# Optimization experiments

Hardware: AMD Instinct MI355X
Metric: run time of the kernel (lower is better)

The kernel has to match this reference:

```python
import jax, jax.numpy as jnp
import numpy as np

LSTM_SIZE = 512
MEM_SIZE = 2048
MEM_DIM = 256
NB_READS = 4
GAMMA = 0.95
EPS = 1e-8
B = 64
IN_RAW = 256
IN_TOTAL = IN_RAW + NB_READS * MEM_SIZE  # 8448
PARAM_DIM = (2 * MEM_DIM + 1) * NB_READS  # 2052


def setup_inputs() -> dict:
    key = jax.random.key(0)
    ks = jax.random.split(key, 8)
    s = 0.02
    return {
        "x": jax.random.normal(ks[0], (B, IN_RAW), jnp.float32),
        "M": jax.random.normal(ks[1], (B, MEM_SIZE, MEM_DIM), jnp.float32),
        "wu": jax.random.uniform(ks[2], (B, MEM_SIZE), jnp.float32),
        "wr": jax.random.uniform(ks[3], (B, NB_READS * MEM_SIZE), jnp.float32),
        "h0": jnp.zeros((LSTM_SIZE,), jnp.float32),
        "c0": jnp.zeros((LSTM_SIZE,), jnp.float32),
        "W_ih": jax.random.normal(ks[4], (4 * LSTM_SIZE, IN_TOTAL), jnp.float32) * s,
        "W_hh": jax.random.normal(ks[5], (4 * LSTM_SIZE, LSTM_SIZE), jnp.float32) * s,
        "b_ih": jnp.zeros((4 * LSTM_SIZE,), jnp.float32),
        "b_hh": jnp.zeros((4 * LSTM_SIZE,), jnp.float32),
        "W_p": jax.random.normal(ks[6], (PARAM_DIM, LSTM_SIZE), jnp.float32) * s,
        "b_p": jax.random.uniform(ks[7], (PARAM_DIM,), jnp.float32, -0.1, 0.1),
    }


def _lstm_scan(x_seq, h0, c0, W_ih, W_hh, b):
    # torch treats the 2-D input as an unbatched sequence of length B:
    # the recurrence runs across the batch axis with a single shared state.
    xW = x_seq @ W_ih.T + b  # [B, 4H] precomputed input contribution

    def step(carry, xw):
        h, c = carry
        g = xw + h @ W_hh.T
        i, f, gg, o = jnp.split(g, 4)
        c = jax.nn.sigmoid(f) * c + jax.nn.sigmoid(i) * jnp.tanh(gg)
        h = jax.nn.sigmoid(o) * jnp.tanh(c)
        return (h, c), h

    (hf, cf), hs = jax.lax.scan(step, (h0, c0), xW)
    return hs, hf, cf


def reference(x, M, wu, wr, h0, c0, W_ih, W_hh, b_ih, b_hh, W_p, b_p):
    ctrl_in = jnp.concatenate([x, wr], axis=-1)  # [B, IN_TOTAL]
    hs, hf, cf = _lstm_scan(ctrl_in, h0, c0, W_ih, W_hh, b_ih + b_hh)
    param = hs @ W_p.T + b_p  # [B, PARAM_DIM]

    nd = NB_READS * MEM_DIM
    k = jnp.tanh(param[:, :nd]).reshape(B, NB_READS, MEM_DIM)
    a = jnp.tanh(param[:, nd:2 * nd]).reshape(B, NB_READS, MEM_DIM)
    sig_alpha = jax.nn.sigmoid(param[:, -NB_READS:])  # [B, R]

    # least_used: topk(wu, k=MEM_SIZE) == full descending sort of indices
    order = jnp.argsort(-wu, axis=-1)  # [B, MEM_SIZE]
    lu_idx = order[:, -1]  # least used slot
    wlu = jax.nn.one_hot(order[:, -NB_READS:], MEM_SIZE, dtype=M.dtype).sum(1)  # [B, N]

    # read head addressing: cosine similarity softmax
    ip = jnp.einsum('brd,bnd->brn', k, M)  # [B, R, N]
    k_norm = jnp.sqrt(jnp.sum(k * k, -1))[:, :, None]
    M_norm = jnp.sqrt(jnp.sum(M * M, -1))[:, None, :]
    wr_t = jax.nn.softmax(ip / (k_norm * M_norm + EPS), axis=-1)  # [B, R, N]

    # write head addressing
    wr_prev3 = wr.reshape(B, NB_READS, MEM_SIZE)
    sa = sig_alpha[:, :, None]
    ww_t = sa * wr_prev3 + (1.0 - sa) * wlu[:, None, :]  # [B, R, N]

    wu_t = GAMMA * wu + wr_t.sum(1) + ww_t.sum(1)  # [B, N]

    erase = 1.0 - jax.nn.one_hot(lu_idx, MEM_SIZE, dtype=M.dtype)  # [B, N]
    M_t = M * erase[:, :, None] + jnp.einsum('brn,brd->bnd', ww_t, a)  # [B, N, D]
    r_t = jnp.einsum('brn,bnd->brd', wr_t, M_t).reshape(B, nd)  # [B, R*D]

    return jnp.concatenate([hs, r_t], axis=-1)  # [B, LSTM+R*D]
```

## Files before the change

### kernel.cpp

```cpp
#include <hip/hip_runtime.h>
#include <hip/hip_bf16.h>

#define BB 64
#define IN_RAW_ 256
#define KIN_ 8448
#define WRW 8192
#define PD_ 2052
#define XW_KS 11
#define XW_CH 768

__global__ __launch_bounds__(256) void k_xw_partial(
    const float* __restrict__ x, const float* __restrict__ wr,
    const float* __restrict__ Wih, float* __restrict__ xwp) {
  const int jb = blockIdx.x & 31;
  const int ks = blockIdx.x >> 5;
  const int j0 = jb << 6;
  const int k0 = ks * XW_CH;
  __shared__ __align__(16) float As[32][68];
  __shared__ __align__(16) float Bs[32][68];
  const int tid = threadIdx.x;
  const int ti = tid & 15, tj = tid >> 4;
  const int lt = tid >> 2, lq = tid & 3;
  float acc[4][4];
#pragma unroll
  for (int i = 0; i < 4; ++i)
#pragma unroll
    for (int j = 0; j < 4; ++j) acc[i][j] = 0.f;
  for (int kc = 0; kc < XW_CH; kc += 32) {
    __syncthreads();
    const int kb = k0 + kc + (lq << 3);
    float va[8], vb[8];
    if (kb < IN_RAW_) {
      const float* p = x + lt * IN_RAW_ + kb;
#pragma unroll
      for (int u = 0; u < 8; ++u) va[u] = p[u];
    } else {
      const float* p = wr + (size_t)lt * WRW + (kb - IN_RAW_);
#pragma unroll
      for (int u = 0; u < 8; ++u) va[u] = p[u];
    }
    {
      const float* p = Wih + (size_t)(j0 + lt) * KIN_ + kb;
#pragma unroll
      for (int u = 0; u < 8; ++u) vb[u] = p[u];
    }
#pragma unroll
    for (int u = 0; u < 8; ++u) As[(lq << 3) + u][lt] = va[u];
#pragma unroll
    for (int u = 0; u < 8; ++u) Bs[(lq << 3) + u][lt] = vb[u];
    __syncthreads();
#pragma unroll
    for (int kk = 0; kk < 32; ++kk) {
      const float4 a4 = *(const float4*)&As[kk][ti << 2];
      const float4 b4 = *(const float4*)&Bs[kk][tj << 2];
      const float av[4] = {a4.x, a4.y, a4.z, a4.w};
      const float bv[4] = {b4.x, b4.y, b4.z, b4.w};
#pragma unroll
      for (int i = 0; i < 4; ++i)
#pragma unroll
        for (int j = 0; j < 4; ++j) acc[i][j] = fmaf(av[i], bv[j], acc[i][j]);
    }
  }
#pragma unroll
  for (int i = 0; i < 4; ++i) {
    const int t = (ti << 2) + i;
    float* dst = xwp + ((size_t)(ks * BB + t) << 11) + j0 + (tj << 2);
    dst[0] = acc[i][0]; dst[1] = acc[i][1]; dst[2] = acc[i][2]; dst[3] = acc[i][3];
  }
}

__global__ __launch_bounds__(256) void k_xw_reduce(
    const float* __restrict__ xwp, const float* __restrict__ bih,
    const float* __restrict__ bhh, float* __restrict__ xw) {
  const int e = blockIdx.x * 256 + threadIdx.x;
  const int j = e & 2047;
  float s = bih[j] + bhh[j];
#pragma unroll
  for (int ks = 0; ks < XW_KS; ++ks) s += xwp[(size_t)ks * 131072 + e];
  xw[e] = s;
}

__global__ __launch_bounds__(64, 1) void k_scan(
    const float* __restrict__ xw, const float* __restrict__ Whh,
    const float* __restrict__ h0, const float* __restrict__ c0,
    unsigned long long* __restrict__ ht, float* __restrict__ out,
    const float* __restrict__ wu, int* __restrict__ t4) {
  const int W = blockIdx.x;
  const int l = threadIdx.x;
  if (W >= 128) {
    const int b = W - 128;
    float val[32];
#pragma unroll
    for (int i = 0; i < 32; ++i) val[i] = wu[(b << 11) + (i << 6) + l];
    for (int pick = 0; pick < 4; ++pick) {
      float bv = 3.4e38f; int bi = -1;
#pragma unroll
      for (int i = 0; i < 32; ++i) {
        const int n = (i << 6) + l;
        const float v = val[i];
        if (v < bv || (v == bv && n > bi)) { bv = v; bi = n; }
      }
#pragma unroll
      for (int s = 1; s < 64; s <<= 1) {
        const float ov = __shfl_xor(bv, s);
        const int oi = __shfl_xor(bi, s);
        if (ov < bv || (ov == bv && oi > bi)) { bv = ov; bi = oi; }
      }
      if (l == 0) t4[(b << 2) + pick] = bi;
      if ((bi & 63) == l) val[bi >> 6] = 3.4e38f;
    }
    return;
  }
  const int d = l & 3;
  const int jj = (W << 2) + d;
  float wreg[16][8];
#pragma unroll
  for (int r = 0; r < 16; ++r) {
    const int row = ((r >> 2) << 9) + (W << 2) + (r & 3);
    const float* p = Whh + ((size_t)row << 9) + (l << 3);
#pragma unroll
    for (int u = 0; u < 8; ++u) wreg[r][u] = p[u];
  }
  float c = 0.f;
  if (l < 4) c = c0[jj];
  float h[8];
#pragma unroll
  for (int u = 0; u < 8; ++u) h[u] = h0[(l << 3) + u];

  for (int t = 0; t < 64; ++t) {
    float xv0 = 0, xv1 = 0, xv2 = 0, xv3 = 0;
    if (l < 4) {
      const float* xp = xw + (t << 11) + jj;
      xv0 = xp[0]; xv1 = xp[512]; xv2 = xp[1024]; xv3 = xp[1536];
    }
    if (t > 0) {
      const unsigned long long* hp = ht + (t << 9) + (l << 3);
      unsigned long long va[8], vb[8];
#pragma unroll
      for (int u = 0; u < 8; ++u)
        va[u] = __hip_atomic_load(hp + u, __ATOMIC_RELAXED, __HIP_MEMORY_SCOPE_AGENT);
      for (;;) {
#pragma unroll
        for (int u = 0; u < 8; ++u)
          vb[u] = __hip_atomic_load(hp + u, __ATOMIC_RELAXED, __HIP_MEMORY_SCOPE_AGENT);
        bool ra = true;
#pragma unroll
        for (int u = 0; u < 8; ++u) ra &= ((unsigned)(va[u] >> 32) == (unsigned)t);
        if (ra) break;
#pragma unroll
        for (int u = 0; u < 8; ++u)
          va[u] = __hip_atomic_load(hp + u, __ATOMIC_RELAXED, __HIP_MEMORY_SCOPE_AGENT);
        bool rb_ = true;
#pragma unroll
        for (int u = 0; u < 8; ++u) rb_ &= ((unsigned)(vb[u] >> 32) == (unsigned)t);
        if (rb_) {
#pragma unroll
          for (int u = 0; u < 8; ++u) va[u] = vb[u];
          break;
        }
      }
#pragma unroll
      for (int u = 0; u < 8; ++u) h[u] = __uint_as_float((unsigned)va[u]);
    }
    float pr[16];
#pragma unroll
    for (int r = 0; r < 16; ++r) {
      float s = 0.f;
#pragma unroll
      for (int u = 0; u < 8; ++u) s = fmaf(wreg[r][u], h[u], s);
      pr[r] = s;
    }
    float v8[8], v4[4], v2[2], v1;
    {
      const bool b0 = (l & 1) != 0;
#pragma unroll
      for (int j = 0; j < 8; ++j) {
        const float keep = b0 ? pr[2 * j + 1] : pr[2 * j];
        const float send = b0 ? pr[2 * j] : pr[2 * j + 1];
        v8[j] = keep + __shfl_xor(send, 1);
      }
    }
    {
      const bool b1 = (l & 2) != 0;
#pragma unroll
      for (int j = 0; j < 4; ++j) {
        const float keep = b1 ? v8[2 * j + 1] : v8[2 * j];
        const float send = b1 ? v8[2 * j] : v8[2 * j + 1];
        v4[j] = keep + __shfl_xor(send, 2);
      }
    }
    {
      const bool b2 = (l & 4) != 0;
#pragma unroll
      for (int j = 0; j < 2; ++j) {
        const float keep = b2 ? v4[2 * j + 1] : v4[2 * j];
        const float send = b2 ? v4[2 * j] : v4[2 * j + 1];
        v2[j] = keep + __shfl_xor(send, 4);
      }
    }
    {
      const bool b3 = (l & 8) != 0;
      const float keep = b3 ? v2[1] : v2[0];
      const float send = b3 ? v2[0] : v2[1];
      v1 = keep + __shfl_xor(send, 8);
    }
    v1 += __shfl_xor(v1, 16);
    v1 += __shfl_xor(v1, 32);
    const float gi_ = __shfl(v1, d);
    const float gf_ = __shfl(v1, d + 4);
    const float gg_ = __shfl(v1, d + 8);
    const float go_ = __shfl(v1, d + 12);
    if (l < 4) {
      const float gi = gi_ + xv0;
      const float gf = gf_ + xv1;
      const float gg = gg_ + xv2;
      const float go = go_ + xv3;
      const float si = 1.f / (1.f + __expf(-gi));
      const float sf = 1.f / (1.f + __expf(-gf));
      const float so = 1.f / (1.f + __expf(-go));
      const float tg = 2.f / (1.f + __expf(-2.f * gg)) - 1.f;
      c = sf * c + si * tg;
      const float tc = 2.f / (1.f + __expf(-2.f * c)) - 1.f;
      const float hnew = so * tc;
      const unsigned long long pk =
          ((unsigned long long)(unsigned)(t + 1) << 32) |
          (unsigned long long)__float_as_uint(hnew);
      __hip_atomic_store(ht + ((t + 1) << 9) + jj, pk, __ATOMIC_RELAXED,
                         __HIP_MEMORY_SCOPE_AGENT);
      out[t * 1536 + jj] = hnew;
    }
  }
}

__global__ __launch_bounds__(256) void k_param(
    const float* __restrict__ outbuf, const float* __restrict__ Wp,
    const float* __restrict__ bp, float* __restrict__ km,
    float* __restrict__ am, float* __restrict__ sa) {
  const int j0 = blockIdx.x << 6;
  __shared__ __align__(16) float As[32][68];
  __shared__ __align__(16) float Bs[32][68];
  const int tid = threadIdx.x;
  const int ti = tid & 15, tj = tid >> 4;
  const int lt = tid >> 2, lq = tid & 3;
  float acc[4][4];
#pragma unroll
  for (int i = 0; i < 4; ++i)
#pragma unroll
    for (int j = 0; j < 4; ++j) acc[i][j] = 0.f;
  for (int kc = 0; kc < 512; kc += 32) {
    __syncthreads();
    const int kb = kc + (lq << 3);
    float va[8], vb[8];
    {
      const float* p = outbuf + lt * 1536 + kb;
#pragma unroll
      for (int u = 0; u < 8; ++u) va[u] = p[u];
    }
    const int brow = j0 + lt;
    if (brow < PD_) {
      const float* p = Wp + (size_t)brow * 512 + kb;
#pragma unroll
      for (int u = 0; u < 8; ++u) vb[u] = p[u];
    } else {
#pragma unroll
      for (int u = 0; u < 8; ++u) vb[u] = 0.f;
    }
#pragma unroll
    for (int u = 0; u < 8; ++u) As[(lq << 3) + u][lt] = va[u];
#pragma unroll
    for (int u = 0; u < 8; ++u) Bs[(lq << 3) + u][lt] = vb[u];
    __syncthreads();
#pragma unroll
    for (int kk = 0; kk < 32; ++kk) {
      const float4 a4 = *(const float4*)&As[kk][ti << 2];
      const float4 b4 = *(const float4*)&Bs[kk][tj << 2];
      const float av[4] = {a4.x, a4.y, a4.z, a4.w};
      const float bv[4] = {b4.x, b4.y, b4.z, b4.w};
#pragma unroll
      for (int i = 0; i < 4; ++i)
#pragma unroll
        for (int j = 0; j < 4; ++j) acc[i][j] = fmaf(av[i], bv[j], acc[i][j]);
    }
  }
#pragma unroll
  for (int i = 0; i < 4; ++i) {
    const int b = (ti << 2) + i;
#pragma unroll
    for (int j = 0; j < 4; ++j) {
      const int col = j0 + (tj << 2) + j;
      if (col < PD_) {
        const float v = acc[i][j] + bp[col];
        if (col < 1024) km[(b << 10) + col] = tanhf(v);
        else if (col < 2048) am[(b << 10) + col - 1024] = tanhf(v);
        else sa[(b << 2) + col - 2048] = 1.f / (1.f + expf(-v));
      }
    }
  }
}

__global__ __launch_bounds__(256) void k_ip(
    const float* __restrict__ M, const float* __restrict__ km,
    float* __restrict__ ip, float* __restrict__ mn) {
  const int b = blockIdx.x >> 4;
  const int nb = blockIdx.x & 15;
  const int n0 = nb << 7;
  const int tid = threadIdx.x;
  const int wv = tid >> 6, l = tid & 63;
  const int q = l >> 4, l16 = l & 15;
  float kr[4][16];
#pragma unroll
  for (int r = 0; r < 4; ++r)
#pragma unroll
    for (int cc = 0; cc < 4; ++cc) {
      const float4 kv = *(const float4*)(km + (((b << 2) + r) << 8) + (cc << 6) + (l16 << 2));
      kr[r][(cc << 2) + 0] = kv.x; kr[r][(cc << 2) + 1] = kv.y;
      kr[r][(cc << 2) + 2] = kv.z; kr[r][(cc << 2) + 3] = kv.w;
    }
  for (int it = 0; it < 8; ++it) {
    const int n = n0 + (wv << 5) + (it << 2) + q;
    const float* mrow = M + (((size_t)b << 11) + n) * 256;
    float s[4] = {0.f, 0.f, 0.f, 0.f};
    float sm = 0.f;
#pragma unroll
    for (int cc = 0; cc < 4; ++cc) {
      const float4 m4 = *(const float4*)(mrow + (cc << 6) + (l16 << 2));
      const float mv[4] = {m4.x, m4.y, m4.z, m4.w};
#pragma unroll
      for (int e = 0; e < 4; ++e) {
        sm = fmaf(mv[e], mv[e], sm);
#pragma unroll
        for (int r = 0; r < 4; ++r) s[r] = fmaf(kr[r][(cc << 2) + e], mv[e], s[r]);
      }
    }
#pragma unroll
    for (int r = 0; r < 4; ++r) {
      float v = s[r];
      v += __shfl_xor(v, 1); v += __shfl_xor(v, 2); v += __shfl_xor(v, 4); v += __shfl_xor(v, 8);
      s[r] = v;
    }
    sm += __shfl_xor(sm, 1); sm += __shfl_xor(sm, 2); sm += __shfl_xor(sm, 4); sm += __shfl_xor(sm, 8);
    if (l16 == 0) {
      const size_t base = ((size_t)b) << 13;
      ip[base + n] = s[0];
      ip[base + 2048 + n] = s[1];
      ip[base + 4096 + n] = s[2];
      ip[base + 6144 + n] = s[3];
      mn[(b << 11) + n] = sqrtf(sm);
    }
  }
}

__global__ __launch_bounds__(512) void k_softmax(
    const float* __restrict__ ip, const float* __restrict__ mn_g,
    const float* __restrict__ sa_g, const float* __restrict__ wr_in,
    const int* __restrict__ t4, const float* __restrict__ am,
    const float* __restrict__ M, const float* __restrict__ km,
    float* __restrict__ wrt, float* __restrict__ rb) {
  const int b = blockIdx.x;
  const int tid = threadIdx.x;
  const int wv = tid >> 6, l = tid & 63;
  __shared__ float lam[4][2048];
  __shared__ float mnl[2048];
  __shared__ float Sd[16];
  __shared__ float t4s[4];
  __shared__ float Sl[16];
#pragma unroll
  for (int i = 0; i < 4; ++i) mnl[tid + (i << 9)] = mn_g[(b << 11) + tid + (i << 9)];
  __syncthreads();
  if (wv < 4) {
    const int r = wv;
    const float* kp = km + (b << 10) + (r << 8);
    float sq = 0.f;
#pragma unroll
    for (int i = 0; i < 4; ++i) { const float v = kp[l + (i << 6)]; sq = fmaf(v, v, sq); }
    sq += __shfl_xor(sq, 1);  sq += __shfl_xor(sq, 2);  sq += __shfl_xor(sq, 4);
    sq += __shfl_xor(sq, 8);  sq += __shfl_xor(sq, 16); sq += __shfl_xor(sq, 32);
    const float kn = sqrtf(sq);
    const float* ipr = ip + (((size_t)b) << 13) + ((size_t)r << 11);
    float mx = -3.4e38f;
#pragma unroll 4
    for (int i = 0; i < 32; ++i) {
      const int n = l + (i << 6);
      const float v = ipr[n] / fmaf(kn, mnl[n], 1e-8f);
      lam[r][n] = v;
      mx = fmaxf(mx, v);
    }
    mx = fmaxf(mx, __shfl_xor(mx, 1));  mx = fmaxf(mx, __shfl_xor(mx, 2));
    mx = fmaxf(mx, __shfl_xor(mx, 4));  mx = fmaxf(mx, __shfl_xor(mx, 8));
    mx = fmaxf(mx, __shfl_xor(mx, 16)); mx = fmaxf(mx, __shfl_xor(mx, 32));
    float sum = 0.f;
#pragma unroll 4
    for (int i = 0; i < 32; ++i) {
      const int n = l + (i << 6);
      const float e = expf(lam[r][n] - mx);
      lam[r][n] = e;
      sum += e;
    }
    sum += __shfl_xor(sum, 1);  sum += __shfl_xor(sum, 2);  sum += __shfl_xor(sum, 4);
    sum += __shfl_xor(sum, 8);  sum += __shfl_xor(sum, 16); sum += __shfl_xor(sum, 32);
    const float inv = 1.f / sum;
#pragma unroll 4
    for (int i = 0; i < 32; ++i) {
      const int n = l + (i << 6);
      const float w_ = lam[r][n] * inv;
      lam[r][n] = w_;
      wrt[(((size_t)(b << 2) + r) << 11) + n] = w_;
    }
  }
  __syncthreads();
#pragma unroll
  for (int j = 0; j < 2; ++j) {
    const int pr = (wv << 1) + j;
    const int r = pr >> 2, qq = pr & 3;
    const float* wp = wr_in + (size_t)b * WRW + (qq << 11);
    float s = 0.f;
#pragma unroll 4
    for (int i = 0; i < 32; ++i) {
      const int n = l + (i << 6);
      s = fmaf(lam[r][n], wp[n], s);
    }
    s += __shfl_xor(s, 1);  s += __shfl_xor(s, 2);  s += __shfl_xor(s, 4);
    s += __shfl_xor(s, 8);  s += __shfl_xor(s, 16); s += __shfl_xor(s, 32);
    if (l == 0) Sd[pr] = s;
  }
  if (tid < 4) {
    float s = 0.f;
#pragma unroll
    for (int ii = 0; ii < 4; ++ii) s += lam[tid][t4[(b << 2) + ii]];
    t4s[tid] = s;
  }
  __syncthreads();
  if (tid < 16) {
    const int r = tid >> 2, qq = tid & 3;
    const float sv = sa_g[(b << 2) + qq];
    Sl[tid] = sv * Sd[tid] + (1.f - sv) * t4s[r];
  }
  __syncthreads();
  const int luv = t4[b << 2];
#pragma unroll
  for (int i = 0; i < 2; ++i) {
    const int e = tid + (i << 9);
    const int r = e >> 8, d = e & 255;
    const float mlu = M[(((size_t)b << 11) + luv) * 256 + d];
    float v = -lam[r][luv] * mlu;
#pragma unroll
    for (int qq = 0; qq < 4; ++qq)
      v = fmaf(Sl[(r << 2) + qq], am[(((b << 2) + qq) << 8) + d], v);
    rb[(((b << 2) + r) << 8) + d] = v;
  }
}

__global__ __launch_bounds__(256) void k_rt_partial(
    const float* __restrict__ wrt, const float* __restrict__ M,
    float* __restrict__ rtp) {
  const int b = blockIdx.x >> 3;
  const int ns = blockIdx.x & 7;
  const int tid = threadIdx.x;
  const int wv = tid >> 6, l = tid & 63;
  __shared__ float wl[4][256];
  __shared__ float4 red[4][4][64];
#pragma unroll
  for (int i = 0; i < 4; ++i) {
    const int e = tid + (i << 8);
    const int r = e >> 8, nn = e & 255;
    wl[r][nn] = wrt[(((size_t)(b << 2) + r) << 11) + (ns << 8) + nn];
  }
  __syncthreads();
  float4 acc[4];
#pragma unroll
  for (int r = 0; r < 4; ++r) acc[r] = make_float4(0.f, 0.f, 0.f, 0.f);
  for (int it = 0; it < 64; ++it) {
    const int nl = (wv << 6) + it;
    const float4 m4 =
        *(const float4*)(M + (((size_t)b << 11) + (ns << 8) + nl) * 256 + (l << 2));
#pragma unroll
    for (int r = 0; r < 4; ++r) {
      const float w_ = wl[r][nl];
      acc[r].x = fmaf(w_, m4.x, acc[r].x);
      acc[r].y = fmaf(w_, m4.y, acc[r].y);
      acc[r].z = fmaf(w_, m4.z, acc[r].z);
      acc[r].w = fmaf(w_, m4.w, acc[r].w);
    }
  }
#pragma unroll
  for (int r = 0; r < 4; ++r) red[wv][r][l] = acc[r];
  __syncthreads();
  if (wv == 0) {
#pragma unroll
    for (int r = 0; r < 4; ++r) {
      float4 s = red[0][r][l];
#pragma unroll
      for (int w2 = 1; w2 < 4; ++w2) {
        const float4 o = red[w2][r][l];
        s.x += o.x; s.y += o.y; s.z += o.z; s.w += o.w;
      }
      *(float4*)(rtp + ((size_t)(((ns << 6) + b) << 2) + r) * 256 + (l << 2)) = s;
    }
  }
}

__global__ __launch_bounds__(256) void k_rt_finish(
    const float* __restrict__ rtp, const float* __restrict__ rb,
    float* __restrict__ out) {
  const int b = blockIdx.x;
  const int tid = threadIdx.x;
#pragma unroll
  for (int i = 0; i < 4; ++i) {
    const int e = tid + (i << 8);
    float s = rb[(b << 10) + e];
#pragma unroll
    for (int ns = 0; ns < 8; ++ns) s += rtp[((size_t)(((ns << 6) + b)) << 10) + e];
    out[b * 1536 + 512 + e] = s;
  }
}

extern "C" void kernel_launch(void* const* d_in, const int* in_sizes, int n_in,
                              void* d_out, int out_size, void* d_ws, size_t ws_size,
                              hipStream_t stream) {
  (void)in_sizes; (void)n_in; (void)out_size;
  const float* x   = (const float*)d_in[0];
  const float* M   = (const float*)d_in[1];
  const float* wu  = (const float*)d_in[2];
  const float* wr  = (const float*)d_in[3];
  const float* h0  = (const float*)d_in[4];
  const float* c0  = (const float*)d_in[5];
  const float* Wih = (const float*)d_in[6];
  const float* Whh = (const float*)d_in[7];
  const float* bih = (const float*)d_in[8];
  const float* bhh = (const float*)d_in[9];
  const float* Wp  = (const float*)d_in[10];
  const float* bp  = (const float*)d_in[11];
  float* out = (float*)d_out;
  char* ws = (char*)d_ws;
  if (ws_size < 14161920u) return;

  float* xwp = (float*)(ws + 0);
  float* xw  = (float*)(ws + 5767168);
  float* km  = (float*)(ws + 6291456);
  float* am  = (float*)(ws + 6553600);
  float* sa  = (float*)(ws + 6815744);
  int*   t4  = (int*)(ws + 6816768);
  float* ipb = (float*)(ws + 6817792);
  float* mnb = (float*)(ws + 8914944);
  float* wrt = (float*)(ws + 9439232);
  float* rb  = (float*)(ws + 11536384);
  float* rtp = (float*)(ws + 11798528);
  unsigned long long* ht = (unsigned long long*)(ws + 13895680);

  hipMemsetAsync(ht, 0, 65 * 512 * 8, stream);
  hipLaunchKernelGGL(k_xw_partial, dim3(352), dim3(256), 0, stream, x, wr, Wih, xwp);
  hipLaunchKernelGGL(k_xw_reduce, dim3(512), dim3(256), 0, stream, xwp, bih, bhh, xw);
  hipLaunchKernelGGL(k_scan, dim3(192), dim3(64), 0, stream,
                     xw, Whh, h0, c0, ht, out, wu, t4);
  hipLaunchKernelGGL(k_param, dim3(33), dim3(256), 0, stream, out, Wp, bp, km, am, sa);
  hipLaunchKernelGGL(k_ip, dim3(1024), dim3(256), 0, stream, M, km, ipb, mnb);
  hipLaunchKernelGGL(k_softmax, dim3(64), dim3(512), 0, stream,
                     ipb, mnb, sa, wr, t4, am, M, km, wrt, rb);
  hipLaunchKernelGGL(k_rt_partial, dim3(512), dim3(256), 0, stream, wrt, M, rtp);
  hipLaunchKernelGGL(k_rt_finish, dim3(64), dim3(256), 0, stream, rtp, rb, out);
}
```

Measured before the change: 284.5 us.

## Move memory-norm computation into scan side blocks and fuse readout into softmax

The per-slot memory norms are now computed by 256 extra blocks launched alongside the sequential LSTM scan kernel, so that work hides under the latency-bound recurrence instead of sitting in k_ip. The softmax kernel now also performs the weighted read over M directly from shared-memory weights and writes the output. This removes the wrt/rb/rtp intermediates and two kernel launches. The risk is that the fused readout runs with only 64 blocks, each streaming 2 MB of M, which may underuse the GPU compared with the earlier 512-block split. The extra scan blocks could also contend with the scan's spin-synchronising blocks.

```diff
diff --git a/kernel.cpp b/kernel.cpp
--- a/kernel.cpp
+++ b/kernel.cpp
@@ -84,9 +84,30 @@
     const float* __restrict__ xw, const float* __restrict__ Whh,
     const float* __restrict__ h0, const float* __restrict__ c0,
     unsigned long long* __restrict__ ht, float* __restrict__ out,
-    const float* __restrict__ wu, int* __restrict__ t4) {
+    const float* __restrict__ wu, int* __restrict__ t4,
+    const float* __restrict__ M, float* __restrict__ mn) {
   const int W = blockIdx.x;
   const int l = threadIdx.x;
+  if (W >= 192) {
+    const int idx = W - 192;
+    const int g0 = idx << 9;
+    const int sub = l >> 4, c16 = l & 15;
+    for (int it = 0; it < 128; ++it) {
+      const int g = g0 + (it << 2) + sub;
+      const float* mrow = M + (size_t)g * 256;
+      float sq = 0.f;
+#pragma unroll
+      for (int ch = 0; ch < 4; ++ch) {
+        const float4 m4 = *(const float4*)(mrow + (ch << 6) + (c16 << 2));
+        sq = fmaf(m4.x, m4.x, sq); sq = fmaf(m4.y, m4.y, sq);
+        sq = fmaf(m4.z, m4.z, sq); sq = fmaf(m4.w, m4.w, sq);
+      }
+      sq += __shfl_xor(sq, 1); sq += __shfl_xor(sq, 2);
+      sq += __shfl_xor(sq, 4); sq += __shfl_xor(sq, 8);
+      if (c16 == 0) mn[g] = sqrtf(sq);
+    }
+    return;
+  }
   if (W >= 128) {
     const int b = W - 128;
     float val[32];
@@ -300,7 +321,7 @@
 
 __global__ __launch_bounds__(256) void k_ip(
     const float* __restrict__ M, const float* __restrict__ km,
-    float* __restrict__ ip, float* __restrict__ mn) {
+    float* __restrict__ ip) {
   const int b = blockIdx.x >> 4;
   const int nb = blockIdx.x & 15;
   const int n0 = nb << 7;
@@ -320,14 +341,12 @@
     const int n = n0 + (wv << 5) + (it << 2) + q;
     const float* mrow = M + (((size_t)b << 11) + n) * 256;
     float s[4] = {0.f, 0.f, 0.f, 0.f};
-    float sm = 0.f;
 #pragma unroll
     for (int cc = 0; cc < 4; ++cc) {
       const float4 m4 = *(const float4*)(mrow + (cc << 6) + (l16 << 2));
       const float mv[4] = {m4.x, m4.y, m4.z, m4.w};
 #pragma unroll
       for (int e = 0; e < 4; ++e) {
-        sm = fmaf(mv[e], mv[e], sm);
 #pragma unroll
         for (int r = 0; r < 4; ++r) s[r] = fmaf(kr[r][(cc << 2) + e], mv[e], s[r]);
       }
@@ -338,24 +357,22 @@
       v += __shfl_xor(v, 1); v += __shfl_xor(v, 2); v += __shfl_xor(v, 4); v += __shfl_xor(v, 8);
       s[r] = v;
     }
-    sm += __shfl_xor(sm, 1); sm += __shfl_xor(sm, 2); sm += __shfl_xor(sm, 4); sm += __shfl_xor(sm, 8);
     if (l16 == 0) {
       const size_t base = ((size_t)b) << 13;
       ip[base + n] = s[0];
       ip[base + 2048 + n] = s[1];
       ip[base + 4096 + n] = s[2];
       ip[base + 6144 + n] = s[3];
-      mn[(b << 11) + n] = sqrtf(sm);
-    }
-  }
-}
-
-__global__ __launch_bounds__(512) void k_softmax(
+    }
+  }
+}
+
+__global__ __launch_bounds__(512) void k_smrt(
     const float* __restrict__ ip, const float* __restrict__ mn_g,
     const float* __restrict__ sa_g, const float* __restrict__ wr_in,
     const int* __restrict__ t4, const float* __restrict__ am,
     const float* __restrict__ M, const float* __restrict__ km,
-    float* __restrict__ wrt, float* __restrict__ rb) {
+    float* __restrict__ out) {
   const int b = blockIdx.x;
   const int tid = threadIdx.x;
   const int wv = tid >> 6, l = tid & 63;
@@ -364,6 +381,7 @@
   __shared__ float Sd[16];
   __shared__ float t4s[4];
   __shared__ float Sl[16];
+  __shared__ float wlu4[4];
 #pragma unroll
   for (int i = 0; i < 4; ++i) mnl[tid + (i << 9)] = mn_g[(b << 11) + tid + (i << 9)];
   __syncthreads();
@@ -402,9 +420,7 @@
 #pragma unroll 4
     for (int i = 0; i < 32; ++i) {
       const int n = l + (i << 6);
-      const float w_ = lam[r][n] * inv;
-      lam[r][n] = w_;
-      wrt[(((size_t)(b << 2) + r) << 11) + n] = w_;
+      lam[r][n] *= inv;
     }
   }
   __syncthreads();
@@ -428,6 +444,7 @@
 #pragma unroll
     for (int ii = 0; ii < 4; ++ii) s += lam[tid][t4[(b << 2) + ii]];
     t4s[tid] = s;
+    wlu4[tid] = lam[tid][t4[b << 2]];
   }
   __syncthreads();
   if (tid < 16) {
@@ -436,80 +453,41 @@
     Sl[tid] = sv * Sd[tid] + (1.f - sv) * t4s[r];
   }
   __syncthreads();
-  const int luv = t4[b << 2];
-#pragma unroll
-  for (int i = 0; i < 2; ++i) {
-    const int e = tid + (i << 9);
-    const int r = e >> 8, d = e & 255;
-    const float mlu = M[(((size_t)b << 11) + luv) * 256 + d];
-    float v = -lam[r][luv] * mlu;
-#pragma unroll
-    for (int qq = 0; qq < 4; ++qq)
-      v = fmaf(Sl[(r << 2) + qq], am[(((b << 2) + qq) << 8) + d], v);
-    rb[(((b << 2) + r) << 8) + d] = v;
-  }
-}
-
-__global__ __launch_bounds__(256) void k_rt_partial(
-    const float* __restrict__ wrt, const float* __restrict__ M,
-    float* __restrict__ rtp) {
-  const int b = blockIdx.x >> 3;
-  const int ns = blockIdx.x & 7;
-  const int tid = threadIdx.x;
-  const int wv = tid >> 6, l = tid & 63;
-  __shared__ float wl[4][256];
-  __shared__ float4 red[4][4][64];
-#pragma unroll
-  for (int i = 0; i < 4; ++i) {
-    const int e = tid + (i << 8);
-    const int r = e >> 8, nn = e & 255;
-    wl[r][nn] = wrt[(((size_t)(b << 2) + r) << 11) + (ns << 8) + nn];
-  }
-  __syncthreads();
   float4 acc[4];
 #pragma unroll
   for (int r = 0; r < 4; ++r) acc[r] = make_float4(0.f, 0.f, 0.f, 0.f);
-  for (int it = 0; it < 64; ++it) {
-    const int nl = (wv << 6) + it;
-    const float4 m4 =
-        *(const float4*)(M + (((size_t)b << 11) + (ns << 8) + nl) * 256 + (l << 2));
+  const float* Mb = M + (((size_t)b << 11)) * 256;
+#pragma unroll 4
+  for (int it = 0; it < 256; ++it) {
+    const int n = (wv << 8) + it;
+    const float4 m4 = *(const float4*)(Mb + (size_t)n * 256 + (l << 2));
 #pragma unroll
     for (int r = 0; r < 4; ++r) {
-      const float w_ = wl[r][nl];
+      const float w_ = lam[r][n];
       acc[r].x = fmaf(w_, m4.x, acc[r].x);
       acc[r].y = fmaf(w_, m4.y, acc[r].y);
       acc[r].z = fmaf(w_, m4.z, acc[r].z);
       acc[r].w = fmaf(w_, m4.w, acc[r].w);
     }
   }
-#pragma unroll
-  for (int r = 0; r < 4; ++r) red[wv][r][l] = acc[r];
   __syncthreads();
-  if (wv == 0) {
-#pragma unroll
-    for (int r = 0; r < 4; ++r) {
-      float4 s = red[0][r][l];
-#pragma unroll
-      for (int w2 = 1; w2 < 4; ++w2) {
-        const float4 o = red[w2][r][l];
-        s.x += o.x; s.y += o.y; s.z += o.z; s.w += o.w;
-      }
-      *(float4*)(rtp + ((size_t)(((ns << 6) + b) << 2) + r) * 256 + (l << 2)) = s;
-    }
-  }
-}
-
-__global__ __launch_bounds__(256) void k_rt_finish(
-    const float* __restrict__ rtp, const float* __restrict__ rb,
-    float* __restrict__ out) {
-  const int b = blockIdx.x;
-  const int tid = threadIdx.x;
-#pragma unroll
-  for (int i = 0; i < 4; ++i) {
-    const int e = tid + (i << 8);
-    float s = rb[(b << 10) + e];
-#pragma unroll
-    for (int ns = 0; ns < 8; ++ns) s += rtp[((size_t)(((ns << 6) + b)) << 10) + e];
+  float* red = &lam[0][0];
+#pragma unroll
+  for (int r = 0; r < 4; ++r)
+    *(float4*)(red + (((wv << 2) + r) << 8) + (l << 2)) = acc[r];
+  __syncthreads();
+  const int luv = t4[b << 2];
+#pragma unroll
+  for (int i = 0; i < 2; ++i) {
+    const int e = tid + (i << 9);
+    const int r = e >> 8, d = e & 255;
+    float s = -wlu4[r] * M[(((size_t)b << 11) + luv) * 256 + d];
+#pragma unroll
+    for (int qq = 0; qq < 4; ++qq)
+      s = fmaf(Sl[(r << 2) + qq], am[(((b << 2) + qq) << 8) + d], s);
+#pragma unroll
+    for (int w2 = 0; w2 < 8; ++w2)
+      s += red[(((w2 << 2) + r) << 8) + d];
     out[b * 1536 + 512 + e] = s;
   }
 }
@@ -532,7 +510,7 @@
   const float* bp  = (const float*)d_in[11];
   float* out = (float*)d_out;
   char* ws = (char*)d_ws;
-  if (ws_size < 14161920u) return;
+  if (ws_size < 9705472u) return;
 
   float* xwp = (float*)(ws + 0);
   float* xw  = (float*)(ws + 5767168);
@@ -542,20 +520,15 @@
   int*   t4  = (int*)(ws + 6816768);
   float* ipb = (float*)(ws + 6817792);
   float* mnb = (float*)(ws + 8914944);
-  float* wrt = (float*)(ws + 9439232);
-  float* rb  = (float*)(ws + 11536384);
-  float* rtp = (float*)(ws + 11798528);
-  unsigned long long* ht = (unsigned long long*)(ws + 13895680);
+  unsigned long long* ht = (unsigned long long*)(ws + 9439232);
 
   hipMemsetAsync(ht, 0, 65 * 512 * 8, stream);
   hipLaunchKernelGGL(k_xw_partial, dim3(352), dim3(256), 0, stream, x, wr, Wih, xwp);
   hipLaunchKernelGGL(k_xw_reduce, dim3(512), dim3(256), 0, stream, xwp, bih, bhh, xw);
-  hipLaunchKernelGGL(k_scan, dim3(192), dim3(64), 0, stream,
-                     xw, Whh, h0, c0, ht, out, wu, t4);
+  hipLaunchKernelGGL(k_scan, dim3(448), dim3(64), 0, stream,
+                     xw, Whh, h0, c0, ht, out, wu, t4, M, mnb);
   hipLaunchKernelGGL(k_param, dim3(33), dim3(256), 0, stream, out, Wp, bp, km, am, sa);
-  hipLaunchKernelGGL(k_ip, dim3(1024), dim3(256), 0, stream, M, km, ipb, mnb);
-  hipLaunchKernelGGL(k_softmax, dim3(64), dim3(512), 0, stream,
-                     ipb, mnb, sa, wr, t4, am, M, km, wrt, rb);
-  hipLaunchKernelGGL(k_rt_partial, dim3(512), dim3(256), 0, stream, wrt, M, rtp);
-  hipLaunchKernelGGL(k_rt_finish, dim3(64), dim3(256), 0, stream, rtp, rb, out);
-}
+  hipLaunchKernelGGL(k_ip, dim3(1024), dim3(256), 0, stream, M, km, ipb);
+  hipLaunchKernelGGL(k_smrt, dim3(64), dim3(512), 0, stream,
+                     ipb, mnb, sa, wr, t4, am, M, km, out);
+}
```

Result: slower. 293.3 us (+3.1%).
